# Kernel optimization log

Measured on AMD Instinct MI355X. Metric: run time of the kernel, lower is better.

## Reference

```python
import jax, jax.numpy as jnp
import numpy as np

IN_CH, OUT_CH = 32, 32
MX, MY = 16, 16


def setup_inputs() -> dict:
    key = jax.random.key(0)
    kx, k1r, k1i, k2r, k2i = jax.random.split(key, 5)
    scale = 1.0 / (IN_CH * OUT_CH)
    x = jax.random.normal(kx, (16, IN_CH, 256, 256), dtype=jnp.float32)
    w_shape = (IN_CH, OUT_CH, MX, MY)
    # complex weights stored as real/imag float32 pairs (torch.randn(cfloat) draws
    # independent normal real and imaginary parts)
    w1_real = jax.random.normal(k1r, w_shape, dtype=jnp.float32) * scale
    w1_imag = jax.random.normal(k1i, w_shape, dtype=jnp.float32) * scale
    w2_real = jax.random.normal(k2r, w_shape, dtype=jnp.float32) * scale
    w2_imag = jax.random.normal(k2i, w_shape, dtype=jnp.float32) * scale
    return {"x": x, "w1_real": w1_real, "w1_imag": w1_imag,
            "w2_real": w2_real, "w2_imag": w2_imag}


def reference(x, w1_real, w1_imag, w2_real, w2_imag):
    b, c_in, gx, gy = x.shape
    w1 = w1_real + 1j * w1_imag  # [Cin, Cout, MX, MY]
    w2 = w2_real + 1j * w2_imag
    x_ft = jnp.fft.rfft2(x, axes=(-2, -1))  # [B, Cin, gx, gy//2+1] complex
    # fused complex channel mixing over retained modes (replaces Cin*Cout loop)
    top = jnp.einsum('bixy,ioxy->boxy', x_ft[:, :, :MX, :MY], w1)
    bot = jnp.einsum('bixy,ioxy->boxy', x_ft[:, :, -MX:, :MY], w2)
    out_ft = jnp.zeros((b, OUT_CH, gx, gy // 2 + 1), dtype=x_ft.dtype)
    out_ft = out_ft.at[:, :, :MX, :MY].set(top)
    out_ft = out_ft.at[:, :, -MX:, :MY].set(bot)
    return jnp.fft.irfft2(out_ft, s=(gx, gy), axes=(-2, -1)).astype(x.dtype)
```

## Files before the change

kernel.cpp:

```cpp
#include <hip/hip_runtime.h>
#include <math.h>

#define B     16
#define CIN   32
#define COUT  32
#define G     256
#define NSITE 512

__device__ __forceinline__ int swz8(int bid, int nwg) {
    int q = nwg >> 3;
    return (bid & 7) * q + (bid >> 3);
}

__global__ __launch_bounds__(256, 2) void k_fwd(const float* __restrict__ x,
                                                float2* __restrict__ X) {
    __shared__ float2 tw[256];
    __shared__ float tile[32][257];
    __shared__ float2 T[256][17];
    const int t = threadIdx.x;
    {
        double ang = (double)t * (M_PI / 128.0);
        tw[t] = make_float2((float)cos(ang), (float)sin(ang));
    }
    const int img = blockIdx.x;
    const float* xp = x + (size_t)img * (G * G);

    float tr[16], ti[16], wr[16], wi[16], sr[16], si[16];
    #pragma unroll
    for (int k = 0; k < 16; ++k) { tr[k] = 0.f; ti[k] = 0.f; }
    __syncthreads();
    #pragma unroll
    for (int k = 1; k < 16; ++k) { sr[k] = tw[k].x; si[k] = -tw[k].y; }

    float4 rs[8];
    #pragma unroll
    for (int p = 0; p < 8; ++p) {
        int idx = p * 256 + t, nx = idx >> 3, sub = idx & 7, h = sub >> 2, q = sub & 3;
        rs[p] = *reinterpret_cast<const float4*>(xp + (size_t)nx * G + (128 * h + 4 * q));
    }
    #pragma unroll
    for (int p = 0; p < 8; ++p) {
        int idx = p * 256 + t, nx = idx >> 3, sub = idx & 7, h = sub >> 2, q = sub & 3;
        int r = 16 * h + 4 * q;
        tile[r + 0][nx] = rs[p].x; tile[r + 1][nx] = rs[p].y;
        tile[r + 2][nx] = rs[p].z; tile[r + 3][nx] = rs[p].w;
    }
    __syncthreads();

    for (int c = 0; c < 8; ++c) {
        const int m0 = c * 16;
        if (c < 7) {
            #pragma unroll
            for (int p = 0; p < 8; ++p) {
                int idx = p * 256 + t, nx = idx >> 3, sub = idx & 7, h = sub >> 2, q = sub & 3;
                rs[p] = *reinterpret_cast<const float4*>(
                    xp + (size_t)nx * G + (m0 + 16 + 128 * h + 4 * q));
            }
        }
        #pragma unroll
        for (int k = 1; k < 16; ++k) {
            float2 w0 = tw[(k * m0) & 255];
            wr[k] = w0.x; wi[k] = -w0.y;
        }
        #pragma unroll
        for (int e = 0; e < 16; ++e) {
            float x0 = tile[e][t], x1 = tile[16 + e][t];
            float ev = x0 + x1, od = x0 - x1;
            tr[0] += ev;
            #pragma unroll
            for (int k = 1; k < 16; ++k) {
                float s_ = (k & 1) ? od : ev;
                tr[k] = fmaf(s_, wr[k], tr[k]);
                ti[k] = fmaf(s_, wi[k], ti[k]);
                float nr = fmaf(wr[k], sr[k], -wi[k] * si[k]);
                wi[k]   = fmaf(wr[k], si[k],  wi[k] * sr[k]);
                wr[k] = nr;
            }
        }
        __syncthreads();
        if (c < 7) {
            #pragma unroll
            for (int p = 0; p < 8; ++p) {
                int idx = p * 256 + t, nx = idx >> 3, sub = idx & 7, h = sub >> 2, q = sub & 3;
                int r = 16 * h + 4 * q;
                tile[r + 0][nx] = rs[p].x; tile[r + 1][nx] = rs[p].y;
                tile[r + 2][nx] = rs[p].z; tile[r + 3][nx] = rs[p].w;
            }
            __syncthreads();
        }
    }
    #pragma unroll
    for (int k = 0; k < 16; ++k) T[t][k] = make_float2(tr[k], ti[k]);
    __syncthreads();

    const int ky = t & 15, kxg = t >> 4;
    float x1r = 0.f, x1i = 0.f, x2r = 0.f, x2i = 0.f;
    const float sgn = 1.f - 2.f * (float)(kxg & 1);
    const float s1r = tw[kxg].x,      s1i = -tw[kxg].y;
    const float s2r = tw[16 - kxg].x, s2i =  tw[16 - kxg].y;
    for (int c2 = 0; c2 < 4; ++c2) {
        const int nx0 = c2 * 32;
        int e1 = (kxg * nx0) & 255;
        float w1r_ = tw[e1].x, w1i_ = -tw[e1].y;
        int e2 = ((16 - kxg) * nx0) & 255;
        float w2r_ = tw[e2].x, w2i_ = tw[e2].y;
        #pragma unroll
        for (int j = 0; j < 32; ++j) {
            float2 a = T[nx0 + j][ky];
            float2 b = T[128 + nx0 + j][ky];
            float pr = fmaf(sgn, b.x, a.x);
            float pi = fmaf(sgn, b.y, a.y);
            x1r = fmaf(pr, w1r_, fmaf(-pi, w1i_, x1r));
            x1i = fmaf(pr, w1i_, fmaf( pi, w1r_, x1i));
            x2r = fmaf(pr, w2r_, fmaf(-pi, w2i_, x2r));
            x2i = fmaf(pr, w2i_, fmaf( pi, w2r_, x2i));
            float n1 = fmaf(w1r_, s1r, -w1i_ * s1i);
            w1i_     = fmaf(w1r_, s1i,  w1i_ * s1r);
            w1r_ = n1;
            float n2 = fmaf(w2r_, s2r, -w2i_ * s2i);
            w2i_     = fmaf(w2r_, s2i,  w2i_ * s2r);
            w2r_ = n2;
        }
    }
    float2* Xp = X + (size_t)img * NSITE;
    Xp[kxg * 16 + ky]        = make_float2(x1r, x1i);
    Xp[(kxg + 16) * 16 + ky] = make_float2(x2r, x2i);
}

__global__ __launch_bounds__(256) void k_mix(const float2* __restrict__ X,
                                             const float* __restrict__ w1r,
                                             const float* __restrict__ w1i,
                                             const float* __restrict__ w2r,
                                             const float* __restrict__ w2i,
                                             float2* __restrict__ Y) {
    __shared__ float2 Ws[CIN][COUT];
    __shared__ float2 Xs[B][CIN];
    const int t = threadIdx.x;
    const int site = swz8(blockIdx.x, NSITE);
    const int kxi = site >> 4, kky = site & 15;
    const float* wr; const float* wi; int kxl;
    if (kxi < 16) { wr = w1r; wi = w1i; kxl = kxi; }
    else          { wr = w2r; wi = w2i; kxl = kxi - 16; }
    const int wofs = kxl * 16 + kky;
    for (int p = t; p < CIN * COUT; p += 256)
        Ws[p >> 5][p & 31] = make_float2(wr[p * 256 + wofs], wi[p * 256 + wofs]);
    for (int p = t; p < B * CIN; p += 256) {
        int bb = p >> 5, i = p & 31;
        Xs[bb][i] = X[(size_t)(bb * CIN + i) * NSITE + site];
    }
    __syncthreads();
    for (int p = t; p < B * COUT; p += 256) {
        int bb = p >> 5, o = p & 31;
        float yr = 0.f, yi = 0.f;
        #pragma unroll
        for (int i = 0; i < CIN; ++i) {
            float2 xv = Xs[bb][i];
            float2 wv = Ws[i][o];
            yr = fmaf(xv.x, wv.x, fmaf(-xv.y, wv.y, yr));
            yi = fmaf(xv.x, wv.y, fmaf( xv.y, wv.x, yi));
        }
        Y[(size_t)(bb * COUT + o) * NSITE + site] = make_float2(yr, yi);
    }
}

__global__ __launch_bounds__(256, 4) void k_inv(const float2* __restrict__ Y,
                                                float* __restrict__ out) {
    __shared__ float2 tw[256];
    __shared__ __align__(16) float2 Ys[32][16];
    __shared__ __align__(16) float2 U[64][18];
    const int t = threadIdx.x;
    {
        double ang = (double)t * (M_PI / 128.0);
        tw[t] = make_float2((float)cos(ang), (float)sin(ang));
    }
    const int img = blockIdx.x >> 2, Q = blockIdx.x & 3;
    const float2* yp = Y + (size_t)img * NSITE;
    reinterpret_cast<float4*>(Ys)[t] = reinterpret_cast<const float4*>(yp)[t];
    __syncthreads();

    const int nxl = t & 63, kg = t >> 6;
    const int nx = Q * 64 + nxl;
    float ur[4], ui[4];
    #pragma unroll
    for (int j = 0; j < 4; ++j) { ur[j] = 0.f; ui[j] = 0.f; }
    const float str = tw[nx].x, sti = tw[nx].y;
    float wr = 1.f, wi = 0.f;
    #pragma unroll 4
    for (int kxi = 0; kxi < 16; ++kxi) {
        float4 a = reinterpret_cast<const float4*>(Ys[kxi])[2 * kg];
        float4 b = reinterpret_cast<const float4*>(Ys[kxi])[2 * kg + 1];
        ur[0] = fmaf(a.x, wr, fmaf(-a.y, wi, ur[0])); ui[0] = fmaf(a.x, wi, fmaf(a.y, wr, ui[0]));
        ur[1] = fmaf(a.z, wr, fmaf(-a.w, wi, ur[1])); ui[1] = fmaf(a.z, wi, fmaf(a.w, wr, ui[1]));
        ur[2] = fmaf(b.x, wr, fmaf(-b.y, wi, ur[2])); ui[2] = fmaf(b.x, wi, fmaf(b.y, wr, ui[2]));
        ur[3] = fmaf(b.z, wr, fmaf(-b.w, wi, ur[3])); ui[3] = fmaf(b.z, wi, fmaf(b.w, wr, ui[3]));
        float nr = fmaf(wr, str, -wi * sti); wi = fmaf(wr, sti, wi * str); wr = nr;
    }
    {
        int e = (16 * nx) & 255;
        wr = tw[e].x; wi = -tw[e].y;
    }
    #pragma unroll 4
    for (int kxi = 16; kxi < 32; ++kxi) {
        float4 a = reinterpret_cast<const float4*>(Ys[kxi])[2 * kg];
        float4 b = reinterpret_cast<const float4*>(Ys[kxi])[2 * kg + 1];
        ur[0] = fmaf(a.x, wr, fmaf(-a.y, wi, ur[0])); ui[0] = fmaf(a.x, wi, fmaf(a.y, wr, ui[0]));
        ur[1] = fmaf(a.z, wr, fmaf(-a.w, wi, ur[1])); ui[1] = fmaf(a.z, wi, fmaf(a.w, wr, ui[1]));
        ur[2] = fmaf(b.x, wr, fmaf(-b.y, wi, ur[2])); ui[2] = fmaf(b.x, wi, fmaf(b.y, wr, ui[2]));
        ur[3] = fmaf(b.z, wr, fmaf(-b.w, wi, ur[3])); ui[3] = fmaf(b.z, wi, fmaf(b.w, wr, ui[3]));
        float nr = fmaf(wr, str, -wi * sti); wi = fmaf(wr, sti, wi * str); wr = nr;
    }
    #pragma unroll
    for (int j = 0; j < 4; ++j) U[nxl][4 * kg + j] = make_float2(ur[j], ui[j]);
    __syncthreads();

    const int wv = t >> 6, ln = t & 63;
    float tc[16], ts[16];
    #pragma unroll
    for (int k = 1; k < 16; ++k) {
        float2 w = tw[(k * ln) & 255];
        tc[k] = 2.f * w.x; ts[k] = 2.f * w.y;
    }
    float* op = out + (size_t)img * (G * G);
    for (int r = 0; r < 16; ++r) {
        const int rl = wv * 16 + r;
        const int nxg = Q * 64 + rl;
        float4 u[8];
        #pragma unroll
        for (int q = 0; q < 8; ++q)
            u[q] = reinterpret_cast<const float4*>(U[rl])[q];
        #pragma unroll
        for (int nb = 0; nb < 4; ++nb) {
            float acc = u[0].x;
            #pragma unroll
            for (int k = 1; k < 16; ++k) {
                float urk = (k & 1) ? u[k >> 1].z : u[k >> 1].x;
                float uik = (k & 1) ? u[k >> 1].w : u[k >> 1].y;
                const int m = (k * nb) & 3;
                if (m == 0)      acc = fmaf(urk, tc[k], fmaf(-uik, ts[k], acc));
                else if (m == 1) acc = fmaf(-urk, ts[k], fmaf(-uik, tc[k], acc));
                else if (m == 2) acc = fmaf(-urk, tc[k], fmaf( uik, ts[k], acc));
                else             acc = fmaf( urk, ts[k], fmaf( uik, tc[k], acc));
            }
            op[(size_t)nxg * G + nb * 64 + ln] = acc * (1.0f / 65536.0f);
        }
    }
}

extern "C" void kernel_launch(void* const* d_in, const int* in_sizes, int n_in,
                              void* d_out, int out_size, void* d_ws, size_t ws_size,
                              hipStream_t stream) {
    const float* x   = (const float*)d_in[0];
    const float* w1r = (const float*)d_in[1];
    const float* w1i = (const float*)d_in[2];
    const float* w2r = (const float*)d_in[3];
    const float* w2i = (const float*)d_in[4];
    float* out = (float*)d_out;

    float2* X = (float2*)d_ws;
    float2* Y = X + (size_t)B * CIN * NSITE;

    k_fwd<<<dim3(B * CIN),      dim3(256), 0, stream>>>(x, X);
    k_mix<<<dim3(NSITE),        dim3(256), 0, stream>>>(X, w1r, w1i, w2r, w2i, Y);
    k_inv<<<dim3(B * COUT * 4), dim3(256), 0, stream>>>(Y, out);
}
```

Before: 304.9 us.

## Split forward DFT into row and column kernels with precomputed twiddles and transposed layouts

Result: no change. 306.4 us (+0.5%).

```diff
diff --git a/kernel.cpp b/kernel.cpp
--- a/kernel.cpp
+++ b/kernel.cpp
@@ -7,90 +7,119 @@
 #define G     256
 #define NSITE 512
 
-__device__ __forceinline__ int swz8(int bid, int nwg) {
-    int q = nwg >> 3;
-    return (bid & 7) * q + (bid >> 3);
-}
-
-__global__ __launch_bounds__(256, 2) void k_fwd(const float* __restrict__ x,
-                                                float2* __restrict__ X) {
+
+__global__ void k_init(float2* __restrict__ tw) {
+    int t = threadIdx.x;
+    double ang = (double)t * (M_PI / 128.0);
+    tw[t] = make_float2((float)cos(ang), (float)sin(ang));
+}
+
+__global__ __launch_bounds__(256) void k_wt(const float* __restrict__ w1r,
+                                            const float* __restrict__ w1i,
+                                            const float* __restrict__ w2r,
+                                            const float* __restrict__ w2i,
+                                            float2* __restrict__ wt) {
+    __shared__ float2 ts[64][65];
+    const int t = threadIdx.x;
+    const int io0 = blockIdx.x * 64;
+    const int s0  = blockIdx.y * 64;
+    const int half = blockIdx.z;
+    const float* wr = half ? w2r : w1r;
+    const float* wi = half ? w2i : w1i;
+    #pragma unroll
+    for (int j = 0; j < 16; ++j) {
+        int e = j * 256 + t;
+        int iol = e >> 6, sl = e & 63;
+        size_t src = (size_t)(io0 + iol) * 256 + s0 + sl;
+        ts[sl][iol] = make_float2(wr[src], wi[src]);
+    }
+    __syncthreads();
+    #pragma unroll
+    for (int j = 0; j < 16; ++j) {
+        int e = j * 256 + t;
+        int srow = e >> 6, iol = e & 63;
+        wt[(size_t)(half * 256 + s0 + srow) * 1024 + io0 + iol] = ts[srow][iol];
+    }
+}
+
+__global__ __launch_bounds__(256, 6) void k_fwdA(const float* __restrict__ x,
+                                                 const float2* __restrict__ twg,
+                                                 float2* __restrict__ T) {
     __shared__ float2 tw[256];
-    __shared__ float tile[32][257];
-    __shared__ float2 T[256][17];
-    const int t = threadIdx.x;
-    {
-        double ang = (double)t * (M_PI / 128.0);
-        tw[t] = make_float2((float)cos(ang), (float)sin(ang));
-    }
-    const int img = blockIdx.x;
-    const float* xp = x + (size_t)img * (G * G);
-
-    float tr[16], ti[16], wr[16], wi[16], sr[16], si[16];
-    #pragma unroll
-    for (int k = 0; k < 16; ++k) { tr[k] = 0.f; ti[k] = 0.f; }
-    __syncthreads();
-    #pragma unroll
-    for (int k = 1; k < 16; ++k) { sr[k] = tw[k].x; si[k] = -tw[k].y; }
-
-    float4 rs[8];
-    #pragma unroll
-    for (int p = 0; p < 8; ++p) {
-        int idx = p * 256 + t, nx = idx >> 3, sub = idx & 7, h = sub >> 2, q = sub & 3;
-        rs[p] = *reinterpret_cast<const float4*>(xp + (size_t)nx * G + (128 * h + 4 * q));
-    }
-    #pragma unroll
-    for (int p = 0; p < 8; ++p) {
-        int idx = p * 256 + t, nx = idx >> 3, sub = idx & 7, h = sub >> 2, q = sub & 3;
-        int r = 16 * h + 4 * q;
-        tile[r + 0][nx] = rs[p].x; tile[r + 1][nx] = rs[p].y;
-        tile[r + 2][nx] = rs[p].z; tile[r + 3][nx] = rs[p].w;
-    }
+    __shared__ float tile[32][68];
+    const int t = threadIdx.x;
+    tw[t] = twg[t];
+    const int img = blockIdx.x >> 2, q = blockIdx.x & 3;
+    const float* xp = x + (size_t)img * (G * G) + (size_t)(q * 64) * G;
+    const int r = t & 63;
+    const int g = __builtin_amdgcn_readfirstlane(t >> 6);
+    const int kbase = 4 * g;
+    const int rr = (t >> 2) & 63, sg = t & 3;
+
+    float tr0 = 0.f, ti0 = 0.f, tr1 = 0.f, ti1 = 0.f;
+    float tr2 = 0.f, ti2 = 0.f, tr3 = 0.f, ti3 = 0.f;
+
+    float4 f0 = *reinterpret_cast<const float4*>(xp + (size_t)rr * G + 4 * sg);
+    float4 f1 = *reinterpret_cast<const float4*>(xp + (size_t)rr * G + 128 + 4 * sg);
+    tile[4 * sg + 0][rr] = f0.x; tile[4 * sg + 1][rr] = f0.y;
+    tile[4 * sg + 2][rr] = f0.z; tile[4 * sg + 3][rr] = f0.w;
+    tile[16 + 4 * sg + 0][rr] = f1.x; tile[16 + 4 * sg + 1][rr] = f1.y;
+    tile[16 + 4 * sg + 2][rr] = f1.z; tile[16 + 4 * sg + 3][rr] = f1.w;
     __syncthreads();
 
     for (int c = 0; c < 8; ++c) {
         const int m0 = c * 16;
         if (c < 7) {
-            #pragma unroll
-            for (int p = 0; p < 8; ++p) {
-                int idx = p * 256 + t, nx = idx >> 3, sub = idx & 7, h = sub >> 2, q = sub & 3;
-                rs[p] = *reinterpret_cast<const float4*>(
-                    xp + (size_t)nx * G + (m0 + 16 + 128 * h + 4 * q));
-            }
-        }
-        #pragma unroll
-        for (int k = 1; k < 16; ++k) {
-            float2 w0 = tw[(k * m0) & 255];
-            wr[k] = w0.x; wi[k] = -w0.y;
-        }
+            f0 = *reinterpret_cast<const float4*>(xp + (size_t)rr * G + (m0 + 16) + 4 * sg);
+            f1 = *reinterpret_cast<const float4*>(xp + (size_t)rr * G + (m0 + 144) + 4 * sg);
+        }
+        int i0 = ((kbase + 0) * m0) & 255, i1 = ((kbase + 1) * m0) & 255;
+        int i2 = ((kbase + 2) * m0) & 255, i3 = ((kbase + 3) * m0) & 255;
         #pragma unroll
         for (int e = 0; e < 16; ++e) {
-            float x0 = tile[e][t], x1 = tile[16 + e][t];
+            float x0 = tile[e][r], x1 = tile[16 + e][r];
             float ev = x0 + x1, od = x0 - x1;
-            tr[0] += ev;
-            #pragma unroll
-            for (int k = 1; k < 16; ++k) {
-                float s_ = (k & 1) ? od : ev;
-                tr[k] = fmaf(s_, wr[k], tr[k]);
-                ti[k] = fmaf(s_, wi[k], ti[k]);
-                float nr = fmaf(wr[k], sr[k], -wi[k] * si[k]);
-                wi[k]   = fmaf(wr[k], si[k],  wi[k] * sr[k]);
-                wr[k] = nr;
-            }
+            float2 w0 = tw[i0], w1 = tw[i1], w2 = tw[i2], w3 = tw[i3];
+            tr0 = fmaf(ev, w0.x, tr0); ti0 = fmaf(ev, -w0.y, ti0);
+            tr1 = fmaf(od, w1.x, tr1); ti1 = fmaf(od, -w1.y, ti1);
+            tr2 = fmaf(ev, w2.x, tr2); ti2 = fmaf(ev, -w2.y, ti2);
+            tr3 = fmaf(od, w3.x, tr3); ti3 = fmaf(od, -w3.y, ti3);
+            i0 = (i0 + kbase + 0) & 255; i1 = (i1 + kbase + 1) & 255;
+            i2 = (i2 + kbase + 2) & 255; i3 = (i3 + kbase + 3) & 255;
         }
         __syncthreads();
         if (c < 7) {
-            #pragma unroll
-            for (int p = 0; p < 8; ++p) {
-                int idx = p * 256 + t, nx = idx >> 3, sub = idx & 7, h = sub >> 2, q = sub & 3;
-                int r = 16 * h + 4 * q;
-                tile[r + 0][nx] = rs[p].x; tile[r + 1][nx] = rs[p].y;
-                tile[r + 2][nx] = rs[p].z; tile[r + 3][nx] = rs[p].w;
-            }
+            tile[4 * sg + 0][rr] = f0.x; tile[4 * sg + 1][rr] = f0.y;
+            tile[4 * sg + 2][rr] = f0.z; tile[4 * sg + 3][rr] = f0.w;
+            tile[16 + 4 * sg + 0][rr] = f1.x; tile[16 + 4 * sg + 1][rr] = f1.y;
+            tile[16 + 4 * sg + 2][rr] = f1.z; tile[16 + 4 * sg + 3][rr] = f1.w;
             __syncthreads();
         }
     }
-    #pragma unroll
-    for (int k = 0; k < 16; ++k) T[t][k] = make_float2(tr[k], ti[k]);
+    float2* Tp = T + ((size_t)img * 16 + kbase) * G + q * 64;
+    Tp[0 * G + r] = make_float2(tr0, ti0);
+    Tp[1 * G + r] = make_float2(tr1, ti1);
+    Tp[2 * G + r] = make_float2(tr2, ti2);
+    Tp[3 * G + r] = make_float2(tr3, ti3);
+}
+
+__global__ __launch_bounds__(256) void k_fwdB(const float2* __restrict__ T,
+                                              const float2* __restrict__ twg,
+                                              float2* __restrict__ X) {
+    __shared__ float2 tw[256];
+    __shared__ float2 Tl[16][258];
+    const int t = threadIdx.x;
+    tw[t] = twg[t];
+    const int img = blockIdx.x;
+    const float2* Tp = T + (size_t)img * 16 * G;
+    #pragma unroll
+    for (int j = 0; j < 8; ++j) {
+        int e = j * 256 + t;
+        float4 v = reinterpret_cast<const float4*>(Tp)[e];
+        int ky_ = e >> 7, c2 = (e & 127) * 2;
+        Tl[ky_][c2]     = make_float2(v.x, v.y);
+        Tl[ky_][c2 + 1] = make_float2(v.z, v.w);
+    }
     __syncthreads();
 
     const int ky = t & 15, kxg = t >> 4;
@@ -106,8 +135,8 @@
         float w2r_ = tw[e2].x, w2i_ = tw[e2].y;
         #pragma unroll
         for (int j = 0; j < 32; ++j) {
-            float2 a = T[nx0 + j][ky];
-            float2 b = T[128 + nx0 + j][ky];
+            float2 a = Tl[ky][nx0 + j];
+            float2 b = Tl[ky][128 + nx0 + j];
             float pr = fmaf(sgn, b.x, a.x);
             float pi = fmaf(sgn, b.y, a.y);
             x1r = fmaf(pr, w1r_, fmaf(-pi, w1i_, x1r));
@@ -122,40 +151,31 @@
             w2r_ = n2;
         }
     }
-    float2* Xp = X + (size_t)img * NSITE;
-    Xp[kxg * 16 + ky]        = make_float2(x1r, x1i);
-    Xp[(kxg + 16) * 16 + ky] = make_float2(x2r, x2i);
+    X[(size_t)(kxg * 16 + ky) * 512 + img]        = make_float2(x1r, x1i);
+    X[(size_t)((kxg + 16) * 16 + ky) * 512 + img] = make_float2(x2r, x2i);
 }
 
 __global__ __launch_bounds__(256) void k_mix(const float2* __restrict__ X,
-                                             const float* __restrict__ w1r,
-                                             const float* __restrict__ w1i,
-                                             const float* __restrict__ w2r,
-                                             const float* __restrict__ w2i,
+                                             const float2* __restrict__ wt,
                                              float2* __restrict__ Y) {
-    __shared__ float2 Ws[CIN][COUT];
-    __shared__ float2 Xs[B][CIN];
-    const int t = threadIdx.x;
-    const int site = swz8(blockIdx.x, NSITE);
-    const int kxi = site >> 4, kky = site & 15;
-    const float* wr; const float* wi; int kxl;
-    if (kxi < 16) { wr = w1r; wi = w1i; kxl = kxi; }
-    else          { wr = w2r; wi = w2i; kxl = kxi - 16; }
-    const int wofs = kxl * 16 + kky;
-    for (int p = t; p < CIN * COUT; p += 256)
-        Ws[p >> 5][p & 31] = make_float2(wr[p * 256 + wofs], wi[p * 256 + wofs]);
-    for (int p = t; p < B * CIN; p += 256) {
-        int bb = p >> 5, i = p & 31;
-        Xs[bb][i] = X[(size_t)(bb * CIN + i) * NSITE + site];
-    }
-    __syncthreads();
+    __shared__ float2 Ws[CIN * COUT];
+    __shared__ float2 Xs[B * CIN];
+    const int t = threadIdx.x;
+    const int site = blockIdx.x;
+    const float2* wp = wt + (size_t)site * 1024;
+    const float2* xp = X + (size_t)site * 512;
+    reinterpret_cast<float4*>(Ws)[t]       = reinterpret_cast<const float4*>(wp)[t];
+    reinterpret_cast<float4*>(Ws)[t + 256] = reinterpret_cast<const float4*>(wp)[t + 256];
+    if (t < 256) reinterpret_cast<float4*>(Xs)[t] = reinterpret_cast<const float4*>(xp)[t];
+    __syncthreads();
+    #pragma unroll
     for (int p = t; p < B * COUT; p += 256) {
         int bb = p >> 5, o = p & 31;
         float yr = 0.f, yi = 0.f;
         #pragma unroll
         for (int i = 0; i < CIN; ++i) {
-            float2 xv = Xs[bb][i];
-            float2 wv = Ws[i][o];
+            float2 xv = Xs[bb * 32 + i];
+            float2 wv = Ws[i * 32 + o];
             yr = fmaf(xv.x, wv.x, fmaf(-xv.y, wv.y, yr));
             yi = fmaf(xv.x, wv.y, fmaf( xv.y, wv.x, yi));
         }
@@ -164,15 +184,13 @@
 }
 
 __global__ __launch_bounds__(256, 4) void k_inv(const float2* __restrict__ Y,
+                                                const float2* __restrict__ twg,
                                                 float* __restrict__ out) {
     __shared__ float2 tw[256];
     __shared__ __align__(16) float2 Ys[32][16];
     __shared__ __align__(16) float2 U[64][18];
     const int t = threadIdx.x;
-    {
-        double ang = (double)t * (M_PI / 128.0);
-        tw[t] = make_float2((float)cos(ang), (float)sin(ang));
-    }
+    tw[t] = twg[t];
     const int img = blockIdx.x >> 2, Q = blockIdx.x & 3;
     const float2* yp = Y + (size_t)img * NSITE;
     reinterpret_cast<float4*>(Ys)[t] = reinterpret_cast<const float4*>(yp)[t];
@@ -256,10 +274,16 @@
     const float* w2i = (const float*)d_in[4];
     float* out = (float*)d_out;
 
-    float2* X = (float2*)d_ws;
-    float2* Y = X + (size_t)B * CIN * NSITE;
-
-    k_fwd<<<dim3(B * CIN),      dim3(256), 0, stream>>>(x, X);
-    k_mix<<<dim3(NSITE),        dim3(256), 0, stream>>>(X, w1r, w1i, w2r, w2i, Y);
-    k_inv<<<dim3(B * COUT * 4), dim3(256), 0, stream>>>(Y, out);
-}
+    float2* tw = (float2*)d_ws;
+    float2* wt = tw + 512;
+    float2* T  = wt + 512 * 1024;
+    float2* X  = T  + 512 * 16 * 256;
+    float2* Y  = X  + 512 * 512;
+
+    k_init<<<dim3(1),          dim3(256), 0, stream>>>(tw);
+    k_wt  <<<dim3(16, 4, 2),   dim3(256), 0, stream>>>(w1r, w1i, w2r, w2i, wt);
+    k_fwdA<<<dim3(B * CIN * 4), dim3(256), 0, stream>>>(x, tw, T);
+    k_fwdB<<<dim3(B * CIN),    dim3(256), 0, stream>>>(T, tw, X);
+    k_mix <<<dim3(NSITE),      dim3(256), 0, stream>>>(X, wt, Y);
+    k_inv <<<dim3(B * COUT * 4), dim3(256), 0, stream>>>(Y, tw, out);
+}
```
